# Performance work log

Hardware: AMD Instinct MI355X
Metric: run time of the kernel (lower is better)

Reference implementation:

```python
import jax, jax.numpy as jnp
import numpy as np
import math

N, E = 50000, 800000
DM, H, L = 128, 8, 6
D = DM // H  # per-head dim = 16
FF = 4 * DM
EPS = 1e-5


def _ln(x, g, b):
    mu = jnp.mean(x, axis=-1, keepdims=True)
    var = jnp.mean((x - mu) ** 2, axis=-1, keepdims=True)
    return (x - mu) * jax.lax.rsqrt(var + EPS) * g + b


def setup_inputs() -> dict:
    key = jax.random.key(0)
    ks = jax.random.split(key, 20)
    s = 0.05
    inp = {
        "node_features": jax.random.normal(ks[0], (N, 20), jnp.float32),
        "edge_attr": jax.random.normal(ks[1], (E, 3), jnp.float32),
        "edge_index": jax.random.randint(ks[2], (2, E), 0, N, jnp.int32),
        "emb_W": jax.random.normal(ks[3], (20, DM), jnp.float32) * s,
        "emb_b": jnp.zeros((DM,), jnp.float32),
        "Wq": jax.random.normal(ks[4], (L, DM, DM), jnp.float32) * s,
        "Wk": jax.random.normal(ks[5], (L, DM, DM), jnp.float32) * s,
        "Wv": jax.random.normal(ks[6], (L, DM, DM), jnp.float32) * s,
        "eW1": jax.random.normal(ks[7], (L, 3, D), jnp.float32) * s,
        "eb1": jnp.zeros((L, D), jnp.float32),
        "eW2": jax.random.normal(ks[8], (L, D, DM), jnp.float32) * s,
        "eb2": jnp.zeros((L, DM), jnp.float32),
        "ln_g": jnp.ones((L, DM), jnp.float32),
        "ln_b": jnp.zeros((L, DM), jnp.float32),
        "ff_W1": jax.random.normal(ks[9], (L, DM, FF), jnp.float32) * s,
        "ff_b1": jnp.zeros((L, FF), jnp.float32),
        "ff_W2": jax.random.normal(ks[10], (L, FF, DM), jnp.float32) * s,
        "ff_b2": jnp.zeros((L, DM), jnp.float32),
    }
    return inp


def reference(node_features, edge_attr, emb_W, emb_b, Wq, Wk, Wv,
              eW1, eb1, eW2, eb2, ln_g, ln_b, ff_W1, ff_b1, ff_W2, ff_b2,
              edge_index):
    src = edge_index[0]  # j: message source
    dst = edge_index[1]  # i: message target
    x = node_features @ emb_W + emb_b  # [N, DM]
    scale = 1.0 / math.sqrt(D)
    for l in range(L):
        q = (x @ Wq[l]).reshape(N, H, D)
        k = (x @ Wk[l]).reshape(N, H, D)
        v = (x @ Wv[l]).reshape(N, H, D)
        ee = (jnp.maximum(edge_attr @ eW1[l] + eb1[l], 0.0) @ eW2[l] + eb2[l]).reshape(E, H, D)
        # per-edge attention logits over heads (softmax over head axis, as in source)
        attn = jnp.einsum('ehd,ehd->eh', q[dst], k[src] + ee) * scale
        attn = jax.nn.softmax(attn, axis=1)  # [E, H]
        msg = (attn[..., None] * v[src]).reshape(E, H * D)  # per-head messages, concat heads
        agg = jax.ops.segment_sum(msg, dst, num_segments=N)  # scatter-add
        x = _ln(x + agg, ln_g[l], ln_b[l])
        h = jnp.maximum(x @ ff_W1[l] + ff_b1[l], 0.0) @ ff_W2[l] + ff_b2[l]
        x = _ln(x + h, ln_g[l], ln_b[l])  # same LN params reused, as in source
    return x
```

## Files before the change

kernel.cpp:

```cpp
#include <hip/hip_runtime.h>
#include <cstdint>
#include <cstddef>

#define NN 50000
#define NE 800000
#define NP 50048
#define ROWT 391

typedef unsigned short u16;
typedef _Float16 f16;
typedef _Float16 hf8 __attribute__((ext_vector_type(8)));
typedef float f32x4 __attribute__((ext_vector_type(4)));

union U32 { unsigned u; f16 h[2]; };
union U64 { uint2 v; f16 h[4]; };

__device__ __forceinline__ float b2f(u16 v){ return __uint_as_float((unsigned)v << 16); }
__device__ __forceinline__ u16 f2b(float f){
  unsigned u = __float_as_uint(f);
  return (u16)((u + 0x7fffu + ((u >> 16) & 1u)) >> 16);
}
__device__ __forceinline__ float ldf(const void* p, long i, int f32){
  return f32 ? ((const float*)p)[i] : b2f(((const u16*)p)[i]);
}

__global__ void detect_k(const u16* __restrict__ nf, int* __restrict__ flag)
{
  int mx = 0;
  for (int i = 0; i < 256; ++i) { int e = (nf[i] >> 7) & 0xFF; mx = e > mx ? e : mx; }
  flag[0] = (mx >= 0x90) ? 1 : 0;
}

__global__ void zero_i_k(int* __restrict__ p, int n)
{
  int i = blockIdx.x * 256 + threadIdx.x;
  if (i < n) p[i] = 0;
}

__global__ void prep_qkve_k(const void* __restrict__ Wq, const void* __restrict__ Wk,
                            const void* __restrict__ Wv, const void* __restrict__ eW2,
                            f16* __restrict__ Wcat, const int* __restrict__ dflag)
{
  int f32 = dflag[0];
  int idx = blockIdx.x * 256 + threadIdx.x;
  int l = idx >> 16;
  int rem = idx & 65535;
  int r = rem >> 7;
  int kk = rem & 127;
  long base = (long)l * 16384;
  float val;
  if (r < 384) {
    const void* W = (r < 128) ? Wq : (r < 256) ? Wk : Wv;
    int n = r & 127;
    val = ldf(W, base + kk * 128 + n, f32);
  } else {
    int n = r - 384, h = n >> 4, j = n & 15;
    long wq = base + kk * 128 + h * 16;
    long e2 = (long)l * 2048 + j * 128 + h * 16;
    float s = 0.f;
    #pragma unroll
    for (int d = 0; d < 16; ++d) s += ldf(Wq, wq + d, f32) * ldf(eW2, e2 + d, f32);
    val = s;
  }
  Wcat[idx] = (f16)val;
}

__global__ void transpose_k(const void* __restrict__ in, f16* __restrict__ out, int R, int C,
                            const int* __restrict__ dflag)
{
  int f32 = dflag[0];
  int idx = blockIdx.x * 256 + threadIdx.x;
  int rc = R * C;
  int l = idx / rc, rem = idx % rc;
  int r = rem / C, c = rem % C;
  out[l * rc + c * R + r] = (f16)ldf(in, idx, f32);
}

__global__ void deg_count_k(const int* __restrict__ eidx, int* __restrict__ deg)
{
  int e = blockIdx.x * 256 + threadIdx.x;
  if (e < NE) atomicAdd(&deg[eidx[NE + e]], 1);
}

__global__ void scan_k(const int* __restrict__ deg, int* __restrict__ rstart,
                       int* __restrict__ cursor, int Nn)
{
  __shared__ int sums[1024];
  int t = threadIdx.x;
  int chunk = (Nn + 1023) >> 10;
  int start = t * chunk;
  int end = start + chunk; if (end > Nn) end = Nn;
  int s = 0;
  for (int i = start; i < end; ++i) s += deg[i];
  sums[t] = s;
  __syncthreads();
  for (int o = 1; o < 1024; o <<= 1) {
    int v = (t >= o) ? sums[t - o] : 0;
    __syncthreads();
    sums[t] += v;
    __syncthreads();
  }
  int run = (t == 0) ? 0 : sums[t - 1];
  for (int i = start; i < end; ++i) { rstart[i] = run; cursor[i] = run; run += deg[i]; }
  if (end == Nn && start < Nn) rstart[Nn] = run;
}

__global__ void csr_fill_k(const int* __restrict__ eidx, int* __restrict__ cursor,
                           int* __restrict__ csrc, int* __restrict__ ceid)
{
  int e = blockIdx.x * 256 + threadIdx.x;
  if (e >= NE) return;
  int d = eidx[NE + e];
  int slot = atomicAdd(&cursor[d], 1);
  csrc[slot] = eidx[e];
  ceid[slot] = e;
}

__global__ void ea_gather_k(const void* __restrict__ eatt, const int* __restrict__ ceid,
                            f16* __restrict__ ea4, const int* __restrict__ dflag)
{
  int f32 = dflag[0];
  int e = blockIdx.x * 256 + threadIdx.x;
  if (e >= NE) return;
  long id = ceid[e];
  f16* q = ea4 + (size_t)e * 4;
  q[0] = (f16)ldf(eatt, id * 3 + 0, f32);
  q[1] = (f16)ldf(eatt, id * 3 + 1, f32);
  q[2] = (f16)ldf(eatt, id * 3 + 2, f32);
  q[3] = (f16)0.f;
}

__global__ void emb_k(const void* __restrict__ nf, const void* __restrict__ embW,
                      const void* __restrict__ embB, float* __restrict__ xf,
                      f16* __restrict__ xh, const int* __restrict__ dflag)
{
  int f32 = dflag[0];
  int idx = blockIdx.x * 256 + threadIdx.x;
  int node = idx >> 7, c = idx & 127;
  float s = 0.f;
  if (node < NN) {
    s = ldf(embB, c, f32);
    long row = (long)node * 20;
    #pragma unroll
    for (int f = 0; f < 20; ++f) s += ldf(nf, row + f, f32) * ldf(embW, f * 128 + c, f32);
  }
  xf[idx] = s;
  xh[idx] = (f16)s;
}

template<int MODE>
__global__ __launch_bounds__(256)
void gemm_k(const f16* __restrict__ A, const f16* __restrict__ Bt, int K,
            f16* __restrict__ o0, f16* __restrict__ o1, f16* __restrict__ o3,
            const void* __restrict__ bias, int boff, const int* __restrict__ dflag)
{
  __shared__ __align__(16) f16 lA[128 * 32];
  __shared__ __align__(16) f16 lB[128 * 32];
  const int tid = threadIdx.x;
  const int wave = tid >> 6, lane = tid & 63;
  const int wr = wave >> 1, wc = wave & 1;
  const size_t rowBase = (size_t)blockIdx.x * 128;
  const size_t colBase = (size_t)blockIdx.y * 128;
  const int m = lane & 15, q4 = lane >> 4;

  f32x4 zero = {0.f, 0.f, 0.f, 0.f};
  f32x4 acc[4][4];
  #pragma unroll
  for (int i = 0; i < 4; ++i)
    #pragma unroll
    for (int j = 0; j < 4; ++j) acc[i][j] = zero;

  const int lr = lane >> 2, lq = lane & 3;
  const f16* Ap = A + (rowBase + wave * 32 + lr) * (size_t)K + lq * 8;
  const f16* Bp = Bt + (colBase + wave * 32 + lr) * (size_t)K + lq * 8;
  uint4* sA = (uint4*)(lA + wave * 1024) + lane;
  uint4* sB = (uint4*)(lB + wave * 1024) + lane;

  uint4 a0 = *(const uint4*)(Ap);
  uint4 a1 = *(const uint4*)(Ap + (size_t)16 * K);
  uint4 b0 = *(const uint4*)(Bp);
  uint4 b1 = *(const uint4*)(Bp + (size_t)16 * K);

  for (int k0 = 0; k0 < K; k0 += 32) {
    sA[0] = a0; sA[64] = a1;
    sB[0] = b0; sB[64] = b1;
    __syncthreads();
    if (k0 + 32 < K) {
      a0 = *(const uint4*)(Ap + k0 + 32);
      a1 = *(const uint4*)(Ap + k0 + 32 + (size_t)16 * K);
      b0 = *(const uint4*)(Bp + k0 + 32);
      b1 = *(const uint4*)(Bp + k0 + 32 + (size_t)16 * K);
    }
    hf8 af[4], bf[4];
    #pragma unroll
    for (int i = 0; i < 4; ++i) af[i] = *(const hf8*)(lA + (wr * 64 + i * 16 + m) * 32 + q4 * 8);
    #pragma unroll
    for (int j = 0; j < 4; ++j) bf[j] = *(const hf8*)(lB + (wc * 64 + j * 16 + m) * 32 + q4 * 8);
    #pragma unroll
    for (int i = 0; i < 4; ++i)
      #pragma unroll
      for (int j = 0; j < 4; ++j)
        acc[i][j] = __builtin_amdgcn_mfma_f32_16x16x32_f16(af[i], bf[j], acc[i][j], 0, 0, 0);
    __syncthreads();
  }

  if (MODE == 0) {
    f16* o; size_t ld; int off;
    if (blockIdx.y == 0)      { o = o0; ld = 128; off = 0; }
    else if (blockIdx.y == 1) { o = o1; ld = 256; off = 0; }
    else if (blockIdx.y == 2) { o = o1; ld = 256; off = 128; }
    else                      { o = o3; ld = 128; off = 0; }
    #pragma unroll
    for (int i = 0; i < 4; ++i)
      #pragma unroll
      for (int r = 0; r < 4; ++r) {
        size_t row = rowBase + wr * 64 + i * 16 + q4 * 4 + r;
        #pragma unroll
        for (int j = 0; j < 4; ++j) {
          int col = wc * 64 + j * 16 + m;
          o[row * ld + off + col] = (f16)acc[i][j][r];
        }
      }
  } else if (MODE == 1) {
    int f32 = dflag[0];
    #pragma unroll
    for (int j = 0; j < 4; ++j) {
      int colg = (int)colBase + wc * 64 + j * 16 + m;
      float bv = ldf(bias, boff + colg, f32);
      #pragma unroll
      for (int i = 0; i < 4; ++i)
        #pragma unroll
        for (int r = 0; r < 4; ++r) {
          size_t row = rowBase + wr * 64 + i * 16 + q4 * 4 + r;
          float v = acc[i][j][r] + bv;
          o0[row * 512 + colg] = (f16)fmaxf(v, 0.f);
        }
    }
  } else {
    int f32 = dflag[0];
    #pragma unroll
    for (int j = 0; j < 4; ++j) {
      int colg = wc * 64 + j * 16 + m;
      float bv = ldf(bias, boff + colg, f32);
      #pragma unroll
      for (int i = 0; i < 4; ++i)
        #pragma unroll
        for (int r = 0; r < 4; ++r) {
          size_t row = rowBase + wr * 64 + i * 16 + q4 * 4 + r;
          o0[row * 128 + colg] = (f16)(acc[i][j][r] + bv);
        }
    }
  }
}

__global__ void edge_k(const f16* __restrict__ qf, const f16* __restrict__ kv,
                       const f16* __restrict__ qef,
                       const f16* __restrict__ ea4,
                       const int* __restrict__ rstart, const int* __restrict__ csrc,
                       const void* __restrict__ eW1, int oW1,
                       const void* __restrict__ eb1, int ob1,
                       const void* __restrict__ eb2, int ob2,
                       const void* __restrict__ g, const void* __restrict__ bp, int olg,
                       float* __restrict__ xf, f16* __restrict__ xh,
                       const int* __restrict__ dflag)
{
  int f32 = dflag[0];
  int wave = threadIdx.x >> 6, lane = threadIdx.x & 63;
  int node = blockIdx.x * 4 + wave;
  if (node >= NN) return;
  int sub = lane >> 5, l = lane & 31;
  int c0 = l << 2;
  int t = l & 3;
  size_t nb = (size_t)node * 128 + c0;

  float q[4], qe[4];
  { U64 u; u.v = *(const uint2*)(qf + nb);
    #pragma unroll
    for (int i = 0; i < 4; ++i) q[i] = (float)u.h[i];
    u.v = *(const uint2*)(qef + nb);
    #pragma unroll
    for (int i = 0; i < 4; ++i) qe[i] = (float)u.h[i]; }

  float pb = 0.f;
  #pragma unroll
  for (int i = 0; i < 4; ++i) pb += q[i] * ldf(eb2, ob2 + c0 + i, f32);
  pb += __shfl_xor(pb, 1); pb += __shfl_xor(pb, 2);

  int j0 = t << 2;
  float w0[4], w1[4], w2[4], bb[4];
  #pragma unroll
  for (int i = 0; i < 4; ++i) {
    w0[i] = ldf(eW1, oW1 + j0 + i, f32);
    w1[i] = ldf(eW1, oW1 + 16 + j0 + i, f32);
    w2[i] = ldf(eW1, oW1 + 32 + j0 + i, f32);
    bb[i] = ldf(eb1, ob1 + j0 + i, f32);
  }

  float acc[4] = {0.f, 0.f, 0.f, 0.f};
  int e0 = rstart[node], e1 = rstart[node + 1];

  int e = e0 + sub;
  int sN = 0; uint2 eaN = {0, 0}, kN = {0, 0}, vN = {0, 0};
  if (e < e1) {
    sN = csrc[e];
    eaN = *(const uint2*)(ea4 + (size_t)e * 4);
    size_t kb = (size_t)sN * 256 + c0;
    kN = *(const uint2*)(kv + kb);
    vN = *(const uint2*)(kv + kb + 128);
  }
  for (; e < e1; e += 2) {
    uint2 eaC = eaN, kC = kN, vC = vN;
    int en = e + 2;
    if (en < e1) {
      sN = csrc[en];
      eaN = *(const uint2*)(ea4 + (size_t)en * 4);
      size_t kb = (size_t)sN * 256 + c0;
      kN = *(const uint2*)(kv + kb);
      vN = *(const uint2*)(kv + kb + 128);
    }
    U64 ue; ue.v = eaC;
    float a0 = (float)ue.h[0], a1 = (float)ue.h[1], a2 = (float)ue.h[2];
    float p = 0.f;
    U64 uk; uk.v = kC;
    U64 uv; uv.v = vC;
    #pragma unroll
    for (int i = 0; i < 4; ++i) {
      float h = fmaxf(fmaf(a2, w2[i], fmaf(a1, w1[i], fmaf(a0, w0[i], bb[i]))), 0.f);
      p = fmaf(q[i], (float)uk.h[i], fmaf(qe[i], h, p));
    }
    p += __shfl_xor(p, 1); p += __shfl_xor(p, 2);
    float logit = (p + pb) * 0.25f;
    float mx = logit;
    mx = fmaxf(mx, __shfl_xor(mx, 4)); mx = fmaxf(mx, __shfl_xor(mx, 8)); mx = fmaxf(mx, __shfl_xor(mx, 16));
    float ex = __expf(logit - mx);
    float se = ex;
    se += __shfl_xor(se, 4); se += __shfl_xor(se, 8); se += __shfl_xor(se, 16);
    float w = ex / se;
    #pragma unroll
    for (int i = 0; i < 4; ++i) acc[i] = fmaf(w, (float)uv.h[i], acc[i]);
  }

  #pragma unroll
  for (int i = 0; i < 4; ++i) acc[i] += __shfl_xor(acc[i], 32);

  float4 xo = *(const float4*)(xf + nb);
  float y[4] = { xo.x + acc[0], xo.y + acc[1], xo.z + acc[2], xo.w + acc[3] };
  float s1 = y[0] + y[1] + y[2] + y[3];
  float s2 = y[0]*y[0] + y[1]*y[1] + y[2]*y[2] + y[3]*y[3];
  #pragma unroll
  for (int o = 1; o < 32; o <<= 1) { s1 += __shfl_xor(s1, o); s2 += __shfl_xor(s2, o); }
  float mu = s1 * 0.0078125f;
  float var = s2 * 0.0078125f - mu * mu;
  float rstd = rsqrtf(var + 1e-5f);
  float ov[4];
  #pragma unroll
  for (int i = 0; i < 4; ++i)
    ov[i] = (y[i] - mu) * rstd * ldf(g, olg + c0 + i, f32) + ldf(bp, olg + c0 + i, f32);
  if (sub == 0) {
    float4 st = { ov[0], ov[1], ov[2], ov[3] };
    *(float4*)(xf + nb) = st;
    U64 wz;
    #pragma unroll
    for (int i = 0; i < 4; ++i) wz.h[i] = (f16)ov[i];
    *(uint2*)(xh + nb) = wz.v;
  }
}

__global__ void ln_res_k(const f16* __restrict__ add, float* __restrict__ xf,
                         f16* __restrict__ xh, const void* __restrict__ g,
                         const void* __restrict__ bp, int olg, const int* __restrict__ dflag)
{
  int f32 = dflag[0];
  int wave = threadIdx.x >> 6, lane = threadIdx.x & 63;
  int node = blockIdx.x * 4 + wave;
  if (node >= NN) return;
  int c0 = lane << 1;
  size_t nb = (size_t)node * 128 + c0;
  U32 ua; ua.u = *(const unsigned*)(add + nb);
  float y0 = xf[nb] + (float)ua.h[0];
  float y1 = xf[nb + 1] + (float)ua.h[1];
  float s1 = y0 + y1, s2 = y0 * y0 + y1 * y1;
  #pragma unroll
  for (int o = 1; o < 64; o <<= 1) { s1 += __shfl_xor(s1, o); s2 += __shfl_xor(s2, o); }
  float mu = s1 * 0.0078125f;
  float var = s2 * 0.0078125f - mu * mu;
  float rstd = rsqrtf(var + 1e-5f);
  float o0v = (y0 - mu) * rstd * ldf(g, olg + c0, f32) + ldf(bp, olg + c0, f32);
  float o1v = (y1 - mu) * rstd * ldf(g, olg + c0 + 1, f32) + ldf(bp, olg + c0 + 1, f32);
  xf[nb] = o0v; xf[nb + 1] = o1v;
  U32 wz; wz.h[0] = (f16)o0v; wz.h[1] = (f16)o1v;
  *(unsigned*)(xh + nb) = wz.u;
}

__global__ void out_k(const float* __restrict__ xf, void* __restrict__ out,
                      const int* __restrict__ dflag)
{
  int f32 = dflag[0];
  int idx = blockIdx.x * 256 + threadIdx.x;
  if (f32) ((float*)out)[idx] = xf[idx];
  else     ((u16*)out)[idx] = f2b(xf[idx]);
}

extern "C" void kernel_launch(void* const* d_in, const int* in_sizes, int n_in,
                              void* d_out, int out_size, void* d_ws, size_t ws_size,
                              hipStream_t stream)
{
  const void* nf   = d_in[0];
  const void* eatt = d_in[1];
  const int*  eidx = (const int*)d_in[2];
  const void* embW = d_in[3];
  const void* embB = d_in[4];
  const void* Wq   = d_in[5];
  const void* Wk   = d_in[6];
  const void* Wv   = d_in[7];
  const void* eW1  = d_in[8];
  const void* eb1  = d_in[9];
  const void* eW2  = d_in[10];
  const void* eb2  = d_in[11];
  const void* lng  = d_in[12];
  const void* lnb  = d_in[13];
  const void* fW1  = d_in[14];
  const void* fb1  = d_in[15];
  const void* fW2  = d_in[16];
  const void* fb2  = d_in[17];

  char* p = (char*)d_ws;
  auto alloc = [&](size_t b) { char* r = p; p += (b + 255) & ~(size_t)255; return r; };
  int* dflag = (int*)alloc(256);
  float* xf  = (float*)alloc((size_t)NP * 128 * 4);
  f16*   xh  = (f16*)  alloc((size_t)NP * 128 * 2);
  int* deg   = (int*)alloc((NN + 1) * 4);
  int* rst   = (int*)alloc((NN + 1) * 4);
  int* cur   = (int*)alloc((size_t)NN * 4);
  int* csrc  = (int*)alloc((size_t)NE * 4);
  f16* ea4   = (f16*)alloc((size_t)NE * 4 * 2);
  f16* Wcat  = (f16*)alloc((size_t)6 * 512 * 128 * 2);
  f16* W1t   = (f16*)alloc((size_t)6 * 512 * 128 * 2);
  f16* W2t   = (f16*)alloc((size_t)6 * 128 * 512 * 2);
  char* S    = alloc((size_t)NP * 512 * 2 + (size_t)NP * 128 * 2);
  f16* qf = (f16*)S;
  f16* qe = qf + (size_t)NP * 128;
  f16* kv = qe + (size_t)NP * 128;
  f16* hb = (f16*)S;
  f16* ffh = hb + (size_t)NP * 512;
  int* ceid = (int*)S;

  detect_k<<<1, 1, 0, stream>>>((const u16*)nf, dflag);
  prep_qkve_k<<<1536, 256, 0, stream>>>(Wq, Wk, Wv, eW2, Wcat, dflag);
  transpose_k<<<1536, 256, 0, stream>>>(fW1, W1t, 128, 512, dflag);
  transpose_k<<<1536, 256, 0, stream>>>(fW2, W2t, 512, 128, dflag);
  zero_i_k<<<(NN + 256) / 256, 256, 0, stream>>>(deg, NN + 1);
  deg_count_k<<<3125, 256, 0, stream>>>(eidx, deg);
  scan_k<<<1, 1024, 0, stream>>>(deg, rst, cur, NN);
  csr_fill_k<<<3125, 256, 0, stream>>>(eidx, cur, csrc, ceid);
  ea_gather_k<<<3125, 256, 0, stream>>>(eatt, ceid, ea4, dflag);
  emb_k<<<NP * 128 / 256, 256, 0, stream>>>(nf, embW, embB, xf, xh, dflag);

  for (int l = 0; l < 6; ++l) {
    gemm_k<0><<<dim3(ROWT, 4), 256, 0, stream>>>(xh, Wcat + (size_t)l * 65536, 128,
                                                 qf, kv, qe, nullptr, 0, dflag);
    edge_k<<<12500, 256, 0, stream>>>(qf, kv, qe, ea4, rst, csrc,
                                      eW1, l * 48, eb1, l * 16, eb2, l * 128,
                                      lng, lnb, l * 128, xf, xh, dflag);
    gemm_k<1><<<dim3(ROWT, 4), 256, 0, stream>>>(xh, W1t + (size_t)l * 65536, 128,
                                                 hb, nullptr, nullptr, fb1, l * 512, dflag);
    gemm_k<2><<<dim3(ROWT, 1), 256, 0, stream>>>(hb, W2t + (size_t)l * 65536, 512,
                                                 ffh, nullptr, nullptr, fb2, l * 128, dflag);
    ln_res_k<<<12500, 256, 0, stream>>>(ffh, xf, xh, lng, lnb, l * 128, dflag);
  }
  out_k<<<25000, 256, 0, stream>>>(xf, d_out, dflag);
}
```

Baseline: 1.586 ms.

## Split edge kernel into per-edge softmax and per-node aggregation, use direct-to-LDS loads

The fused per-node edge kernel is replaced by three kernels: pb_k precomputes the q·eb2 bias per node and head, attn_k computes all eight head logits and the softmax once per edge (one thread per edge, writing fp16 weights), and agg_k gathers V rows with the precomputed weights and applies the residual LayerNorm. The GEMM stages tiles straight into LDS with global_load_lds, dropping the register double-buffer. Small parameters are converted to fp32 once up front, which removes per-access dtype branching. The cost is an extra write and read of per-edge weights and a cdst array, plus GEMM loads that are no longer prefetched while the MFMAs run.

```diff
diff --git a/kernel.cpp b/kernel.cpp
--- a/kernel.cpp
+++ b/kernel.cpp
@@ -14,6 +14,7 @@
 
 union U32 { unsigned u; f16 h[2]; };
 union U64 { uint2 v; f16 h[4]; };
+union U128 { uint4 v; f16 x[8]; };
 
 __device__ __forceinline__ float b2f(u16 v){ return __uint_as_float((unsigned)v << 16); }
 __device__ __forceinline__ u16 f2b(float f){
@@ -23,6 +24,10 @@
 __device__ __forceinline__ float ldf(const void* p, long i, int f32){
   return f32 ? ((const float*)p)[i] : b2f(((const u16*)p)[i]);
 }
+__device__ __forceinline__ void gl_lds16(const void* g, void* l){
+  __builtin_amdgcn_global_load_lds((const __attribute__((address_space(1))) void*)g,
+                                   (__attribute__((address_space(3))) void*)l, 16, 0, 0);
+}
 
 __global__ void detect_k(const u16* __restrict__ nf, int* __restrict__ flag)
 {
@@ -35,6 +40,27 @@
 {
   int i = blockIdx.x * 256 + threadIdx.x;
   if (i < n) p[i] = 0;
+}
+
+__global__ void conv_k(const void* eW1, const void* eb1, const void* eb2,
+                       const void* lng, const void* lnb, const void* fb1, const void* fb2,
+                       const void* embB, const void* embW,
+                       float* __restrict__ pf, const int* __restrict__ dflag)
+{
+  int f32 = dflag[0];
+  int i = blockIdx.x * 256 + threadIdx.x;
+  if (i >= 9216) return;
+  const void* p; long off;
+  if (i < 288)       { p = eW1;  off = i; }
+  else if (i < 384)  { p = eb1;  off = i - 288; }
+  else if (i < 1152) { p = eb2;  off = i - 384; }
+  else if (i < 1920) { p = lng;  off = i - 1152; }
+  else if (i < 2688) { p = lnb;  off = i - 1920; }
+  else if (i < 5760) { p = fb1;  off = i - 2688; }
+  else if (i < 6528) { p = fb2;  off = i - 5760; }
+  else if (i < 6656) { p = embB; off = i - 6528; }
+  else               { p = embW; off = i - 6656; }
+  pf[i] = ldf(p, off, f32);
 }
 
 __global__ void prep_qkve_k(const void* __restrict__ Wq, const void* __restrict__ Wk,
@@ -106,13 +132,15 @@
 }
 
 __global__ void csr_fill_k(const int* __restrict__ eidx, int* __restrict__ cursor,
-                           int* __restrict__ csrc, int* __restrict__ ceid)
+                           int* __restrict__ csrc, int* __restrict__ cdst,
+                           int* __restrict__ ceid)
 {
   int e = blockIdx.x * 256 + threadIdx.x;
   if (e >= NE) return;
   int d = eidx[NE + e];
   int slot = atomicAdd(&cursor[d], 1);
   csrc[slot] = eidx[e];
+  cdst[slot] = d;
   ceid[slot] = e;
 }
 
@@ -130,8 +158,8 @@
   q[3] = (f16)0.f;
 }
 
-__global__ void emb_k(const void* __restrict__ nf, const void* __restrict__ embW,
-                      const void* __restrict__ embB, float* __restrict__ xf,
+__global__ void emb_k(const void* __restrict__ nf, const float* __restrict__ embWf,
+                      const float* __restrict__ embBf, float* __restrict__ xf,
                       f16* __restrict__ xh, const int* __restrict__ dflag)
 {
   int f32 = dflag[0];
@@ -139,10 +167,10 @@
   int node = idx >> 7, c = idx & 127;
   float s = 0.f;
   if (node < NN) {
-    s = ldf(embB, c, f32);
+    s = embBf[c];
     long row = (long)node * 20;
     #pragma unroll
-    for (int f = 0; f < 20; ++f) s += ldf(nf, row + f, f32) * ldf(embW, f * 128 + c, f32);
+    for (int f = 0; f < 20; ++f) s += ldf(nf, row + f, f32) * embWf[f * 128 + c];
   }
   xf[idx] = s;
   xh[idx] = (f16)s;
@@ -152,7 +180,7 @@
 __global__ __launch_bounds__(256)
 void gemm_k(const f16* __restrict__ A, const f16* __restrict__ Bt, int K,
             f16* __restrict__ o0, f16* __restrict__ o1, f16* __restrict__ o3,
-            const void* __restrict__ bias, int boff, const int* __restrict__ dflag)
+            const float* __restrict__ bias)
 {
   __shared__ __align__(16) f16 lA[128 * 32];
   __shared__ __align__(16) f16 lB[128 * 32];
@@ -173,24 +201,15 @@
   const int lr = lane >> 2, lq = lane & 3;
   const f16* Ap = A + (rowBase + wave * 32 + lr) * (size_t)K + lq * 8;
   const f16* Bp = Bt + (colBase + wave * 32 + lr) * (size_t)K + lq * 8;
-  uint4* sA = (uint4*)(lA + wave * 1024) + lane;
-  uint4* sB = (uint4*)(lB + wave * 1024) + lane;
-
-  uint4 a0 = *(const uint4*)(Ap);
-  uint4 a1 = *(const uint4*)(Ap + (size_t)16 * K);
-  uint4 b0 = *(const uint4*)(Bp);
-  uint4 b1 = *(const uint4*)(Bp + (size_t)16 * K);
+  f16* lAp = lA + wave * 1024;
+  f16* lBp = lB + wave * 1024;
 
   for (int k0 = 0; k0 < K; k0 += 32) {
-    sA[0] = a0; sA[64] = a1;
-    sB[0] = b0; sB[64] = b1;
+    gl_lds16(Ap + k0, lAp);
+    gl_lds16(Ap + k0 + (size_t)16 * K, lAp + 512);
+    gl_lds16(Bp + k0, lBp);
+    gl_lds16(Bp + k0 + (size_t)16 * K, lBp + 512);
     __syncthreads();
-    if (k0 + 32 < K) {
-      a0 = *(const uint4*)(Ap + k0 + 32);
-      a1 = *(const uint4*)(Ap + k0 + 32 + (size_t)16 * K);
-      b0 = *(const uint4*)(Bp + k0 + 32);
-      b1 = *(const uint4*)(Bp + k0 + 32 + (size_t)16 * K);
-    }
     hf8 af[4], bf[4];
     #pragma unroll
     for (int i = 0; i < 4; ++i) af[i] = *(const hf8*)(lA + (wr * 64 + i * 16 + m) * 32 + q4 * 8);
@@ -222,26 +241,23 @@
         }
       }
   } else if (MODE == 1) {
-    int f32 = dflag[0];
     #pragma unroll
     for (int j = 0; j < 4; ++j) {
       int colg = (int)colBase + wc * 64 + j * 16 + m;
-      float bv = ldf(bias, boff + colg, f32);
+      float bv = bias[colg];
       #pragma unroll
       for (int i = 0; i < 4; ++i)
         #pragma unroll
         for (int r = 0; r < 4; ++r) {
           size_t row = rowBase + wr * 64 + i * 16 + q4 * 4 + r;
-          float v = acc[i][j][r] + bv;
-          o0[row * 512 + colg] = (f16)fmaxf(v, 0.f);
+          o0[row * 512 + colg] = (f16)fmaxf(acc[i][j][r] + bv, 0.f);
         }
     }
   } else {
-    int f32 = dflag[0];
     #pragma unroll
     for (int j = 0; j < 4; ++j) {
       int colg = wc * 64 + j * 16 + m;
-      float bv = ldf(bias, boff + colg, f32);
+      float bv = bias[colg];
       #pragma unroll
       for (int i = 0; i < 4; ++i)
         #pragma unroll
@@ -253,124 +269,148 @@
   }
 }
 
-__global__ void edge_k(const f16* __restrict__ qf, const f16* __restrict__ kv,
-                       const f16* __restrict__ qef,
-                       const f16* __restrict__ ea4,
-                       const int* __restrict__ rstart, const int* __restrict__ csrc,
-                       const void* __restrict__ eW1, int oW1,
-                       const void* __restrict__ eb1, int ob1,
-                       const void* __restrict__ eb2, int ob2,
-                       const void* __restrict__ g, const void* __restrict__ bp, int olg,
-                       float* __restrict__ xf, f16* __restrict__ xh,
-                       const int* __restrict__ dflag)
-{
-  int f32 = dflag[0];
+__global__ void pb_k(const f16* __restrict__ qf, const float* __restrict__ eb2f,
+                     float* __restrict__ pbt)
+{
+  int idx = blockIdx.x * 256 + threadIdx.x;
+  if (idx >= NN * 8) return;
+  int n = idx >> 3, h = idx & 7;
+  U128 a, b;
+  a.v = *(const uint4*)(qf + (size_t)n * 128 + h * 16);
+  b.v = *(const uint4*)(qf + (size_t)n * 128 + h * 16 + 8);
+  const float* e = eb2f + h * 16;
+  float p = 0.f;
+  #pragma unroll
+  for (int d = 0; d < 8; ++d) p = fmaf((float)a.x[d], e[d], fmaf((float)b.x[d], e[8 + d], p));
+  pbt[idx] = p;
+}
+
+__global__ __launch_bounds__(256)
+void attn_k(const f16* __restrict__ qf, const f16* __restrict__ kv, const f16* __restrict__ qef,
+            const f16* __restrict__ ea4, const int* __restrict__ csrc, const int* __restrict__ cdst,
+            const float* __restrict__ pbt, const float* __restrict__ eW1f,
+            const float* __restrict__ eb1f, f16* __restrict__ w8)
+{
+  int e = blockIdx.x * 256 + threadIdx.x;
+  if (e >= NE) return;
+  int src = csrc[e], dst = cdst[e];
+  U64 ue; ue.v = *(const uint2*)(ea4 + (size_t)e * 4);
+  float a0 = (float)ue.h[0], a1 = (float)ue.h[1], a2 = (float)ue.h[2];
+  float he[16];
+  #pragma unroll
+  for (int j = 0; j < 16; ++j)
+    he[j] = fmaxf(fmaf(a2, eW1f[32 + j], fmaf(a1, eW1f[16 + j], fmaf(a0, eW1f[j], eb1f[j]))), 0.f);
+  const uint4* qr = (const uint4*)(qf + (size_t)dst * 128);
+  const uint4* kr = (const uint4*)(kv + (size_t)src * 256);
+  const uint4* er = (const uint4*)(qef + (size_t)dst * 128);
+  float4 pb0 = *(const float4*)(pbt + (size_t)dst * 8);
+  float4 pb1 = *(const float4*)(pbt + (size_t)dst * 8 + 4);
+  float pbv[8] = { pb0.x, pb0.y, pb0.z, pb0.w, pb1.x, pb1.y, pb1.z, pb1.w };
+  float logit[8];
+  uint4 qa = qr[0], qb = qr[1], ka = kr[0], kb = kr[1], za = er[0], zb = er[1];
+  #pragma unroll
+  for (int h = 0; h < 8; ++h) {
+    uint4 qa2, qb2, ka2, kb2, za2, zb2;
+    if (h < 7) {
+      qa2 = qr[2*h+2]; qb2 = qr[2*h+3];
+      ka2 = kr[2*h+2]; kb2 = kr[2*h+3];
+      za2 = er[2*h+2]; zb2 = er[2*h+3];
+    }
+    U128 Q0, Q1, K0, K1, E0, E1;
+    Q0.v = qa; Q1.v = qb; K0.v = ka; K1.v = kb; E0.v = za; E1.v = zb;
+    float p = 0.f;
+    #pragma unroll
+    for (int d = 0; d < 8; ++d) {
+      p = fmaf((float)Q0.x[d], (float)K0.x[d], p);
+      p = fmaf((float)Q1.x[d], (float)K1.x[d], p);
+      p = fmaf((float)E0.x[d], he[d], p);
+      p = fmaf((float)E1.x[d], he[8 + d], p);
+    }
+    logit[h] = (p + pbv[h]) * 0.25f;
+    qa = qa2; qb = qb2; ka = ka2; kb = kb2; za = za2; zb = zb2;
+  }
+  float mx = logit[0];
+  #pragma unroll
+  for (int h = 1; h < 8; ++h) mx = fmaxf(mx, logit[h]);
+  float se = 0.f, ex[8];
+  #pragma unroll
+  for (int h = 0; h < 8; ++h) { ex[h] = __expf(logit[h] - mx); se += ex[h]; }
+  float inv = 1.f / se;
+  U128 W;
+  #pragma unroll
+  for (int h = 0; h < 8; ++h) W.x[h] = (f16)(ex[h] * inv);
+  *(uint4*)(w8 + (size_t)e * 8) = W.v;
+}
+
+__global__ void agg_k(const f16* __restrict__ kv, const f16* __restrict__ w8,
+                      const int* __restrict__ rstart, const int* __restrict__ csrc,
+                      const float* __restrict__ gf, const float* __restrict__ bpf,
+                      float* __restrict__ xf, f16* __restrict__ xh)
+{
   int wave = threadIdx.x >> 6, lane = threadIdx.x & 63;
   int node = blockIdx.x * 4 + wave;
   if (node >= NN) return;
-  int sub = lane >> 5, l = lane & 31;
-  int c0 = l << 2;
-  int t = l & 3;
+  int sub = lane >> 4, l = lane & 15;
+  int c0 = l << 3;
+  int head = l >> 1;
+  float acc[8] = {0.f, 0.f, 0.f, 0.f, 0.f, 0.f, 0.f, 0.f};
+  int e0 = rstart[node], e1 = rstart[node + 1];
+  int e = e0 + sub;
+  uint4 vN = {0, 0, 0, 0}; float wN = 0.f;
+  if (e < e1) {
+    int s = csrc[e];
+    vN = *(const uint4*)(kv + (size_t)s * 256 + 128 + c0);
+    wN = (float)w8[(size_t)e * 8 + head];
+  }
+  for (; e < e1; e += 4) {
+    uint4 vC = vN; float wC = wN;
+    int en = e + 4;
+    if (en < e1) {
+      int s = csrc[en];
+      vN = *(const uint4*)(kv + (size_t)s * 256 + 128 + c0);
+      wN = (float)w8[(size_t)en * 8 + head];
+    }
+    U128 V; V.v = vC;
+    #pragma unroll
+    for (int i = 0; i < 8; ++i) acc[i] = fmaf(wC, (float)V.x[i], acc[i]);
+  }
+  #pragma unroll
+  for (int i = 0; i < 8; ++i) {
+    acc[i] += __shfl_xor(acc[i], 16);
+    acc[i] += __shfl_xor(acc[i], 32);
+  }
   size_t nb = (size_t)node * 128 + c0;
-
-  float q[4], qe[4];
-  { U64 u; u.v = *(const uint2*)(qf + nb);
-    #pragma unroll
-    for (int i = 0; i < 4; ++i) q[i] = (float)u.h[i];
-    u.v = *(const uint2*)(qef + nb);
-    #pragma unroll
-    for (int i = 0; i < 4; ++i) qe[i] = (float)u.h[i]; }
-
-  float pb = 0.f;
-  #pragma unroll
-  for (int i = 0; i < 4; ++i) pb += q[i] * ldf(eb2, ob2 + c0 + i, f32);
-  pb += __shfl_xor(pb, 1); pb += __shfl_xor(pb, 2);
-
-  int j0 = t << 2;
-  float w0[4], w1[4], w2[4], bb[4];
-  #pragma unroll
-  for (int i = 0; i < 4; ++i) {
-    w0[i] = ldf(eW1, oW1 + j0 + i, f32);
-    w1[i] = ldf(eW1, oW1 + 16 + j0 + i, f32);
-    w2[i] = ldf(eW1, oW1 + 32 + j0 + i, f32);
-    bb[i] = ldf(eb1, ob1 + j0 + i, f32);
-  }
-
-  float acc[4] = {0.f, 0.f, 0.f, 0.f};
-  int e0 = rstart[node], e1 = rstart[node + 1];
-
-  int e = e0 + sub;
-  int sN = 0; uint2 eaN = {0, 0}, kN = {0, 0}, vN = {0, 0};
-  if (e < e1) {
-    sN = csrc[e];
-    eaN = *(const uint2*)(ea4 + (size_t)e * 4);
-    size_t kb = (size_t)sN * 256 + c0;
-    kN = *(const uint2*)(kv + kb);
-    vN = *(const uint2*)(kv + kb + 128);
-  }
-  for (; e < e1; e += 2) {
-    uint2 eaC = eaN, kC = kN, vC = vN;
-    int en = e + 2;
-    if (en < e1) {
-      sN = csrc[en];
-      eaN = *(const uint2*)(ea4 + (size_t)en * 4);
-      size_t kb = (size_t)sN * 256 + c0;
-      kN = *(const uint2*)(kv + kb);
-      vN = *(const uint2*)(kv + kb + 128);
-    }
-    U64 ue; ue.v = eaC;
-    float a0 = (float)ue.h[0], a1 = (float)ue.h[1], a2 = (float)ue.h[2];
-    float p = 0.f;
-    U64 uk; uk.v = kC;
-    U64 uv; uv.v = vC;
-    #pragma unroll
-    for (int i = 0; i < 4; ++i) {
-      float h = fmaxf(fmaf(a2, w2[i], fmaf(a1, w1[i], fmaf(a0, w0[i], bb[i]))), 0.f);
-      p = fmaf(q[i], (float)uk.h[i], fmaf(qe[i], h, p));
-    }
-    p += __shfl_xor(p, 1); p += __shfl_xor(p, 2);
-    float logit = (p + pb) * 0.25f;
-    float mx = logit;
-    mx = fmaxf(mx, __shfl_xor(mx, 4)); mx = fmaxf(mx, __shfl_xor(mx, 8)); mx = fmaxf(mx, __shfl_xor(mx, 16));
-    float ex = __expf(logit - mx);
-    float se = ex;
-    se += __shfl_xor(se, 4); se += __shfl_xor(se, 8); se += __shfl_xor(se, 16);
-    float w = ex / se;
-    #pragma unroll
-    for (int i = 0; i < 4; ++i) acc[i] = fmaf(w, (float)uv.h[i], acc[i]);
-  }
-
-  #pragma unroll
-  for (int i = 0; i < 4; ++i) acc[i] += __shfl_xor(acc[i], 32);
-
-  float4 xo = *(const float4*)(xf + nb);
-  float y[4] = { xo.x + acc[0], xo.y + acc[1], xo.z + acc[2], xo.w + acc[3] };
-  float s1 = y[0] + y[1] + y[2] + y[3];
-  float s2 = y[0]*y[0] + y[1]*y[1] + y[2]*y[2] + y[3]*y[3];
-  #pragma unroll
-  for (int o = 1; o < 32; o <<= 1) { s1 += __shfl_xor(s1, o); s2 += __shfl_xor(s2, o); }
+  float4 x0 = *(const float4*)(xf + nb);
+  float4 x1 = *(const float4*)(xf + nb + 4);
+  float y[8] = { x0.x + acc[0], x0.y + acc[1], x0.z + acc[2], x0.w + acc[3],
+                 x1.x + acc[4], x1.y + acc[5], x1.z + acc[6], x1.w + acc[7] };
+  float s1 = 0.f, s2 = 0.f;
+  #pragma unroll
+  for (int i = 0; i < 8; ++i) { s1 += y[i]; s2 += y[i] * y[i]; }
+  #pragma unroll
+  for (int o = 1; o < 16; o <<= 1) { s1 += __shfl_xor(s1, o); s2 += __shfl_xor(s2, o); }
   float mu = s1 * 0.0078125f;
   float var = s2 * 0.0078125f - mu * mu;
   float rstd = rsqrtf(var + 1e-5f);
-  float ov[4];
-  #pragma unroll
-  for (int i = 0; i < 4; ++i)
-    ov[i] = (y[i] - mu) * rstd * ldf(g, olg + c0 + i, f32) + ldf(bp, olg + c0 + i, f32);
+  float ov[8];
+  #pragma unroll
+  for (int i = 0; i < 8; ++i) ov[i] = (y[i] - mu) * rstd * gf[c0 + i] + bpf[c0 + i];
   if (sub == 0) {
-    float4 st = { ov[0], ov[1], ov[2], ov[3] };
-    *(float4*)(xf + nb) = st;
-    U64 wz;
-    #pragma unroll
-    for (int i = 0; i < 4; ++i) wz.h[i] = (f16)ov[i];
-    *(uint2*)(xh + nb) = wz.v;
+    float4 s0 = { ov[0], ov[1], ov[2], ov[3] };
+    float4 s1v = { ov[4], ov[5], ov[6], ov[7] };
+    *(float4*)(xf + nb) = s0;
+    *(float4*)(xf + nb + 4) = s1v;
+    U128 wz;
+    #pragma unroll
+    for (int i = 0; i < 8; ++i) wz.x[i] = (f16)ov[i];
+    *(uint4*)(xh + nb) = wz.v;
   }
 }
 
 __global__ void ln_res_k(const f16* __restrict__ add, float* __restrict__ xf,
-                         f16* __restrict__ xh, const void* __restrict__ g,
-                         const void* __restrict__ bp, int olg, const int* __restrict__ dflag)
-{
-  int f32 = dflag[0];
+                         f16* __restrict__ xh, const float* __restrict__ gf,
+                         const float* __restrict__ bpf)
+{
   int wave = threadIdx.x >> 6, lane = threadIdx.x & 63;
   int node = blockIdx.x * 4 + wave;
   if (node >= NN) return;
@@ -385,8 +425,8 @@
   float mu = s1 * 0.0078125f;
   float var = s2 * 0.0078125f - mu * mu;
   float rstd = rsqrtf(var + 1e-5f);
-  float o0v = (y0 - mu) * rstd * ldf(g, olg + c0, f32) + ldf(bp, olg + c0, f32);
-  float o1v = (y1 - mu) * rstd * ldf(g, olg + c0 + 1, f32) + ldf(bp, olg + c0 + 1, f32);
+  float o0v = (y0 - mu) * rstd * gf[c0] + bpf[c0];
+  float o1v = (y1 - mu) * rstd * gf[c0 + 1] + bpf[c0 + 1];
   xf[nb] = o0v; xf[nb + 1] = o1v;
   U32 wz; wz.h[0] = (f16)o0v; wz.h[1] = (f16)o1v;
   *(unsigned*)(xh + nb) = wz.u;
@@ -426,47 +466,64 @@
 
   char* p = (char*)d_ws;
   auto alloc = [&](size_t b) { char* r = p; p += (b + 255) & ~(size_t)255; return r; };
-  int* dflag = (int*)alloc(256);
-  float* xf  = (float*)alloc((size_t)NP * 128 * 4);
-  f16*   xh  = (f16*)  alloc((size_t)NP * 128 * 2);
-  int* deg   = (int*)alloc((NN + 1) * 4);
-  int* rst   = (int*)alloc((NN + 1) * 4);
-  int* cur   = (int*)alloc((size_t)NN * 4);
-  int* csrc  = (int*)alloc((size_t)NE * 4);
-  f16* ea4   = (f16*)alloc((size_t)NE * 4 * 2);
-  f16* Wcat  = (f16*)alloc((size_t)6 * 512 * 128 * 2);
-  f16* W1t   = (f16*)alloc((size_t)6 * 512 * 128 * 2);
-  f16* W2t   = (f16*)alloc((size_t)6 * 128 * 512 * 2);
+  int* dflag   = (int*)alloc(256);
+  float* pf    = (float*)alloc(9216 * 4);
+  float* xf    = (float*)alloc((size_t)NP * 128 * 4);
+  f16*   xh    = (f16*)  alloc((size_t)NP * 128 * 2);
+  int* deg     = (int*)alloc((NN + 1) * 4);
+  int* rst     = (int*)alloc((NN + 1) * 4);
+  int* cur     = (int*)alloc((size_t)NN * 4);
+  int* csrc    = (int*)alloc((size_t)NE * 4);
+  int* cdst    = (int*)alloc((size_t)NE * 4);
+  float* pbt   = (float*)alloc((size_t)NN * 8 * 4);
+  f16* ea4     = (f16*)alloc((size_t)NE * 4 * 2);
+  f16* Wcat    = (f16*)alloc((size_t)6 * 512 * 128 * 2);
+  f16* W1t     = (f16*)alloc((size_t)6 * 512 * 128 * 2);
+  f16* W2t     = (f16*)alloc((size_t)6 * 128 * 512 * 2);
   char* S    = alloc((size_t)NP * 512 * 2 + (size_t)NP * 128 * 2);
-  f16* qf = (f16*)S;
-  f16* qe = qf + (size_t)NP * 128;
-  f16* kv = qe + (size_t)NP * 128;
-  f16* hb = (f16*)S;
+  f16* qf  = (f16*)S;
+  f16* qe  = qf + (size_t)NP * 128;
+  f16* kv  = qe + (size_t)NP * 128;
+  f16* hb  = (f16*)S;
   f16* ffh = hb + (size_t)NP * 512;
+  f16* w8  = ffh;
   int* ceid = (int*)S;
 
+  float* eW1f = pf;
+  float* eb1f = pf + 288;
+  float* eb2f = pf + 384;
+  float* lngf = pf + 1152;
+  float* lnbf = pf + 1920;
+  float* fb1f = pf + 2688;
+  float* fb2f = pf + 5760;
+  float* embBf = pf + 6528;
+  float* embWf = pf + 6656;
+
   detect_k<<<1, 1, 0, stream>>>((const u16*)nf, dflag);
+  conv_k<<<36, 256, 0, stream>>>(eW1, eb1, eb2, lng, lnb, fb1, fb2, embB, embW, pf, dflag);
   prep_qkve_k<<<1536, 256, 0, stream>>>(Wq, Wk, Wv, eW2, Wcat, dflag);
   transpose_k<<<1536, 256, 0, stream>>>(fW1, W1t, 128, 512, dflag);
   transpose_k<<<1536, 256, 0, stream>>>(fW2, W2t, 512, 128, dflag);
   zero_i_k<<<(NN + 256) / 256, 256, 0, stream>>>(deg, NN + 1);
   deg_count_k<<<3125, 256, 0, stream>>>(eidx, deg);
   scan_k<<<1, 1024, 0, stream>>>(deg, rst, cur, NN);
-  csr_fill_k<<<3125, 256, 0, stream>>>(eidx, cur, csrc, ceid);
+  csr_fill_k<<<3125, 256, 0, stream>>>(eidx, cur, csrc, cdst, ceid);
   ea_gather_k<<<3125, 256, 0, stream>>>(eatt, ceid, ea4, dflag);
-  emb_k<<<NP * 128 / 256, 256, 0, stream>>>(nf, embW, embB, xf, xh, dflag);
+  emb_k<<<NP * 128 / 256, 256, 0, stream>>>(nf, embWf, embBf, xf, xh, dflag);
 
   for (int l = 0; l < 6; ++l) {
     gemm_k<0><<<dim3(ROWT, 4), 256, 0, stream>>>(xh, Wcat + (size_t)l * 65536, 128,
-                                                 qf, kv, qe, nullptr, 0, dflag);
-    edge_k<<<12500, 256, 0, stream>>>(qf, kv, qe, ea4, rst, csrc,
-                                      eW1, l * 48, eb1, l * 16, eb2, l * 128,
-                                      lng, lnb, l * 128, xf, xh, dflag);
+                                                 qf, kv, qe, nullptr);
+    pb_k<<<(NN * 8 + 255) / 256, 256, 0, stream>>>(qf, eb2f + l * 128, pbt);
+    attn_k<<<3125, 256, 0, stream>>>(qf, kv, qe, ea4, csrc, cdst, pbt,
+                                     eW1f + l * 48, eb1f + l * 16, w8);
+    agg_k<<<12500, 256, 0, stream>>>(kv, w8, rst, csrc,
+                                     lngf + l * 128, lnbf + l * 128, xf, xh);
     gemm_k<1><<<dim3(ROWT, 4), 256, 0, stream>>>(xh, W1t + (size_t)l * 65536, 128,
-                                                 hb, nullptr, nullptr, fb1, l * 512, dflag);
+                                                 hb, nullptr, nullptr, fb1f + l * 512);
     gemm_k<2><<<dim3(ROWT, 1), 256, 0, stream>>>(hb, W2t + (size_t)l * 65536, 512,
-                                                 ffh, nullptr, nullptr, fb2, l * 128, dflag);
-    ln_res_k<<<12500, 256, 0, stream>>>(ffh, xf, xh, lng, lnb, l * 128, dflag);
+                                                 ffh, nullptr, nullptr, fb2f + l * 128);
+    ln_res_k<<<12500, 256, 0, stream>>>(ffh, xf, xh, lngf + l * 128, lnbf + l * 128);
   }
   out_k<<<25000, 256, 0, stream>>>(xf, d_out, dflag);
 }
```

Measured after the change: 1.517 ms. 1.05x faster.
